# Kernel tuning notes

Measured on AMD Instinct MI355X. Metric: run time of the kernel, lower is better.

The kernel has to match this reference:

```python
import jax, jax.numpy as jnp
import numpy as np

RADIUS = 0.2
NUM_POINTS = 32
MAX_POINTS = 60
BN_EPS = 1e-5


def _bn(x, g, b, m, v):
    # BatchNorm in eval mode (running stats), channels-last broadcast
    return g * (x - m) * jax.lax.rsqrt(v + BN_EPS) + b


def setup_inputs() -> dict:
    key = jax.random.key(0)
    nk = lambda i: jax.random.fold_in(key, i)
    B, NQ, NC, HC = 2, 4096, 8192, 64
    inp = {}
    inp['p_query'] = jax.random.uniform(nk(0), (B, NQ, 3), dtype=jnp.float32)
    inp['p_context'] = jax.random.uniform(nk(1), (B, NC, 3), dtype=jnp.float32)
    inp['h_context'] = jax.random.normal(nk(2), (B, NC, HC), dtype=jnp.float32)

    def lin(i, o, ci):
        return (jax.random.normal(nk(i), (o, ci), jnp.float32) / np.sqrt(ci).astype(np.float32),
                0.01 * jax.random.normal(nk(i + 1), (o,), jnp.float32))

    def bnp(i, c):
        return (1.0 + 0.1 * jax.random.normal(nk(i), (c,), jnp.float32),
                0.1 * jax.random.normal(nk(i + 1), (c,), jnp.float32),
                0.1 * jax.random.normal(nk(i + 2), (c,), jnp.float32),
                0.5 + jax.random.uniform(nk(i + 3), (c,), jnp.float32))

    inp['w_xyz'], inp['b_xyz'] = lin(10, 64, 3)
    # pointwise 1x1 Conv2d MLP: 128 -> 128 -> 128 -> 256 (BN after each conv)
    inp['pw_w1'], inp['pw_b1'] = lin(12, 128, 128)
    inp['pw_g1'], inp['pw_be1'], inp['pw_m1'], inp['pw_v1'] = bnp(14, 128)
    inp['pw_w2'], inp['pw_b2'] = lin(20, 128, 128)
    inp['pw_g2'], inp['pw_be2'], inp['pw_m2'], inp['pw_v2'] = bnp(22, 128)
    inp['pw_w3'], inp['pw_b3'] = lin(28, 256, 128)
    inp['pw_g3'], inp['pw_be3'], inp['pw_m3'], inp['pw_v3'] = bnp(30, 256)
    # global 1x1 Conv1d MLP: 256 -> 128 -> 64 -> 3 (BN+ReLU between, none on last)
    inp['g_w1'], inp['g_b1'] = lin(36, 128, 256)
    inp['g_g1'], inp['g_be1'], inp['g_m1'], inp['g_v1'] = bnp(38, 128)
    inp['g_w2'], inp['g_b2'] = lin(44, 64, 128)
    inp['g_g2'], inp['g_be2'], inp['g_m2'], inp['g_v2'] = bnp(46, 64)
    inp['g_w3'], inp['g_b3'] = lin(52, 3, 64)
    return inp


def reference(p_query, p_context, h_context, w_xyz, b_xyz,
              pw_w1, pw_b1, pw_g1, pw_be1, pw_m1, pw_v1,
              pw_w2, pw_b2, pw_g2, pw_be2, pw_m2, pw_v2,
              pw_w3, pw_b3, pw_g3, pw_be3, pw_m3, pw_v3,
              g_w1, g_b1, g_g1, g_be1, g_m1, g_v1,
              g_w2, g_b2, g_g2, g_be2, g_m2, g_v2,
              g_w3, g_b3):
    N = p_context.shape[1]
    # knn_points: squared distances, K smallest sorted ascending
    d = (jnp.sum(p_query ** 2, -1)[:, :, None]
         - 2.0 * jnp.einsum('bqd,bnd->bqn', p_query, p_context)
         + jnp.sum(p_context ** 2, -1)[:, None, :])  # [B,NQ,NC]
    neg, idx = jax.lax.top_k(-d, MAX_POINTS)
    dist = -neg  # [B,NQ,K] ascending
    knn_idx = jnp.where(dist > RADIUS ** 2, N + 1, idx)
    idx = knn_idx[:, :, :NUM_POINTS]
    dist = dist[:, :, :NUM_POINTS]
    mask = idx == N + 1
    idx = jnp.where(mask, 0, idx)
    dist = jnp.where(mask, 0.0, dist)
    gather = jax.vmap(lambda a, i: a[i])
    pts = gather(p_context, idx)        # [B,NQ,P,3]
    h_group = gather(h_context, idx)    # [B,NQ,P,HC]
    p_rel = pts - p_query[:, :, None, :]
    h_rel = p_rel @ w_xyz.T + b_xyz     # Linear(3 -> 64)
    h = jnp.concatenate([h_rel, h_group], -1)  # [B,NQ,P,128]
    h = jax.nn.relu(_bn(h @ pw_w1.T + pw_b1, pw_g1, pw_be1, pw_m1, pw_v1))
    h = jax.nn.relu(_bn(h @ pw_w2.T + pw_b2, pw_g2, pw_be2, pw_m2, pw_v2))
    h = _bn(h @ pw_w3.T + pw_b3, pw_g3, pw_be3, pw_m3, pw_v3)  # [B,NQ,P,256]
    # cosine radius weighting (note: dist is SQUARED distance, faithful to source)
    c = 0.5 * (jnp.cos(dist * (np.pi / RADIUS)) + 1.0)
    c = jnp.where((dist <= RADIUS) & (dist > 0.0), c, 0.0)
    y = jnp.sum(h * c[..., None], axis=2)  # masked weighted pool over neighbors -> [B,NQ,256]
    y = jax.nn.relu(_bn(y @ g_w1.T + g_b1, g_g1, g_be1, g_m1, g_v1))
    y = jax.nn.relu(_bn(y @ g_w2.T + g_b2, g_g2, g_be2, g_m2, g_v2))
    return y @ g_w3.T + g_b3  # [B,NQ,3]
```

## Files before the change

### kernel.cpp

```cpp
#include <hip/hip_runtime.h>
#include <hip/hip_bf16.h>
#include <math.h>

#define BB 2
#define NQ 4096
#define NC 8192
#define KNN 32
#define WCAP 512
#define QB 4
#define MROWS 128
#define BN_EPS 1e-5f

typedef __attribute__((ext_vector_type(8))) short s16x8;
typedef __attribute__((ext_vector_type(4))) float f32x4;

#define WS_IDX   0
#define WS_CW    1048576
#define WS_Z     2097152
#define WS_SQ    6291456
#define WS_PCF   6324224
#define WS_PIDX  6586368
#define WS_CELL  6651904
#define WS_CCNT  6717440
#define WS_COFS  6718464
#define WS_W1    6719488
#define WS_W2    6752256
#define WS_W3    6785024
#define WS_GW1   6850560
#define WS_GW2   6916096
#define WS_F3    6932480
#define WS_FG1   6934528
#define WS_FG2   6935552

__device__ inline int swz(int row, int kbyte, int rb) {
    return row * rb + (kbyte ^ ((row & 7) << 4));
}
__device__ inline unsigned short f2bf(float x) {
    __hip_bfloat16 h = __float2bfloat16(x);
    return *reinterpret_cast<unsigned short*>(&h);
}
__device__ inline float bf2f(unsigned short u) {
    return __uint_as_float(((unsigned)u) << 16);
}
__device__ inline int cell1d(float x) {
    int c = (int)floorf(x * 5.0f);
    return c < 0 ? 0 : (c > 4 ? 4 : c);
}

__device__ inline void mk_img(const float* __restrict__ src, int R, int K, char* dst, int t, int NT)
{
    int rbg = (K * 2) / 16;
    int ng = R * rbg;
    for (int g = t; g < ng; g += NT) {
        int row = g / rbg;
        int b16 = (g - row * rbg) * 16;
        int sb  = b16 ^ ((row & 7) << 4);
        const float* s = src + row * K + sb / 2;
        union { s16x8 v; unsigned short u[8]; } pk;
#pragma unroll
        for (int j = 0; j < 8; ++j) pk.u[j] = f2bf(s[j]);
        *(s16x8*)(dst + row * (K * 2) + b16) = pk.v;
    }
}

__global__ __launch_bounds__(256) void prep_kernel(
    const float* __restrict__ pc,
    const float* __restrict__ w1, const float* __restrict__ w2, const float* __restrict__ w3,
    const float* __restrict__ gw1, const float* __restrict__ gw2,
    const float* __restrict__ g3, const float* __restrict__ b3, const float* __restrict__ m3,
    const float* __restrict__ v3, const float* __restrict__ be3,
    const float* __restrict__ gg1, const float* __restrict__ gb1, const float* __restrict__ gm1,
    const float* __restrict__ gv1, const float* __restrict__ gbe1,
    const float* __restrict__ gg2, const float* __restrict__ gb2, const float* __restrict__ gm2,
    const float* __restrict__ gv2, const float* __restrict__ gbe2,
    char* __restrict__ ws)
{
    const int t = blockIdx.x * 256 + threadIdx.x;
    const int NT = gridDim.x * 256;

    int* cell = (int*)(ws + WS_CELL);
    int* ccnt = (int*)(ws + WS_CCNT);
    for (int i = t; i < BB * NC; i += NT) {
        float x = pc[i*3+0], y = pc[i*3+1], z = pc[i*3+2];
        int c = (cell1d(z)*5 + cell1d(y))*5 + cell1d(x);
        cell[i] = c;
        atomicAdd(&ccnt[(i >> 13)*128 + c], 1);
    }

    mk_img(w1,  128, 128, ws + WS_W1,  t, NT);
    mk_img(w2,  128, 128, ws + WS_W2,  t, NT);
    mk_img(w3,  256, 128, ws + WS_W3,  t, NT);
    mk_img(gw1, 128, 256, ws + WS_GW1, t, NT);
    mk_img(gw2,  64, 128, ws + WS_GW2, t, NT);

    if (t < 256) {
        float s = g3[t] * rsqrtf(v3[t] + BN_EPS);
        ((float2*)(ws + WS_F3))[t] = make_float2(s, s * (b3[t] - m3[t]) + be3[t]);
    }
    if (t < 128) {
        float s = gg1[t] * rsqrtf(gv1[t] + BN_EPS);
        ((float2*)(ws + WS_FG1))[t] = make_float2(s, s * (gb1[t] - gm1[t]) + gbe1[t]);
    }
    if (t < 64) {
        float s = gg2[t] * rsqrtf(gv2[t] + BN_EPS);
        ((float2*)(ws + WS_FG2))[t] = make_float2(s, s * (gb2[t] - gm2[t]) + gbe2[t]);
    }
}

__global__ __launch_bounds__(128) void scan_kernel(char* __restrict__ ws)
{
    int* ccnt = (int*)(ws + WS_CCNT);
    int* cofs = (int*)(ws + WS_COFS);
    const int wv = threadIdx.x >> 6, lane = threadIdx.x & 63;
    const int base = wv * 128;
    int a = (lane < 125) ? ccnt[base + lane] : 0;
    int b = (64 + lane < 125) ? ccnt[base + 64 + lane] : 0;
    int ai = a, bi = b;
    for (int d = 1; d < 64; d <<= 1) {
        int t = __shfl_up(ai, d, 64);
        if (lane >= d) ai += t;
    }
    int totA = __shfl(ai, 63, 64);
    for (int d = 1; d < 64; d <<= 1) {
        int t = __shfl_up(bi, d, 64);
        if (lane >= d) bi += t;
    }
    int exA = ai - a;
    int exB = totA + bi - b;
    cofs[base + lane] = exA;       cofs[base + 64 + lane] = exB;
    ccnt[base + lane] = exA;       ccnt[base + 64 + lane] = exB;
}

__global__ __launch_bounds__(256) void scatter_kernel(
    const float* __restrict__ pc, char* __restrict__ ws)
{
    const int i = blockIdx.x * 256 + threadIdx.x;
    if (i >= BB * NC) return;
    const int b = i >> 13, loc = i & (NC - 1);
    int* cell = (int*)(ws + WS_CELL);
    int* cur  = (int*)(ws + WS_CCNT);
    float4* pcf = (float4*)(ws + WS_PCF);
    int*    pidx = (int*)(ws + WS_PIDX);
    int c = cell[i];
    int pos = atomicAdd(&cur[b*128 + c], 1);
    float x = pc[i*3+0], y = pc[i*3+1], z = pc[i*3+2];
    float w = (x*x + y*y) + z*z;
    pcf[(size_t)b*NC + pos]  = make_float4(x, y, z, w);
    pidx[(size_t)b*NC + pos] = loc;
}

__device__ inline void cmpx64(unsigned long long& k, int& p, int j, bool up) {
    unsigned long long ok = __shfl_xor(k, j, 64);
    int op = __shfl_xor(p, j, 64);
    int lane = threadIdx.x & 63;
    bool lower = (lane & j) == 0;
    bool gt = (k > ok) || (k == ok && p > op);
    bool take = (lower == up) ? gt : !gt;
    if (take) { k = ok; p = op; }
}

__device__ inline void wave_sort128(unsigned long long& k0, int& p0,
                                    unsigned long long& k1, int& p1) {
    const int lane = threadIdx.x & 63;
    for (int kk = 2; kk <= 128; kk <<= 1) {
        for (int j = kk >> 1; j > 0; j >>= 1) {
            if (j == 64) {
                bool sw = (k0 > k1) || (k0 == k1 && p0 > p1);
                if (sw) {
                    unsigned long long tk = k0; k0 = k1; k1 = tk;
                    int tp = p0; p0 = p1; p1 = tp;
                }
            } else {
                bool up0 = ((lane & kk) == 0);
                bool up1 = (kk == 128) ? true : ((kk == 64) ? false : up0);
                cmpx64(k0, p0, j, up0);
                cmpx64(k1, p1, j, up1);
            }
        }
    }
}

__global__ __launch_bounds__(256) void knn_kernel(
    const float* __restrict__ pq, const float* __restrict__ pc,
    const float4* __restrict__ pcf, const int* __restrict__ pidx,
    const int* __restrict__ cofs,
    int* __restrict__ idx_out, float* __restrict__ cw_out)
{
    __shared__ unsigned long long kbuf[4][WCAP];
    __shared__ int pbuf[4][WCAP];

    const int tid = threadIdx.x, lane = tid & 63, w = tid >> 6;
    const int gq = blockIdx.x * 4 + w;
    const int b = gq >> 12;

    const float qxf = pq[gq*3+0], qyf = pq[gq*3+1], qzf = pq[gq*3+2];
    const double qx = (double)qxf, qy = (double)qyf, qz = (double)qzf;
    const double sq = qx*qx + qy*qy + qz*qz;
    const float  sqf = (float)sq;
    const double R2d = 0.2 * 0.2;
    const float  R2f = 0.04f + 1e-4f;

    const float4* pcfb = pcf + (size_t)b * NC;
    const int*    pidb = pidx + (size_t)b * NC;
    const int*    cb   = cofs + b * 128;
    const float*  pcb  = pc + (size_t)b * NC * 3;

    int xlo = (int)floorf((qxf - 0.2f) * 5.0f - 1e-3f); xlo = xlo < 0 ? 0 : xlo;
    int xhi = (int)floorf((qxf + 0.2f) * 5.0f + 1e-3f); xhi = xhi > 4 ? 4 : xhi;
    int ylo = (int)floorf((qyf - 0.2f) * 5.0f - 1e-3f); ylo = ylo < 0 ? 0 : ylo;
    int yhi = (int)floorf((qyf + 0.2f) * 5.0f + 1e-3f); yhi = yhi > 4 ? 4 : yhi;
    int zlo = (int)floorf((qzf - 0.2f) * 5.0f - 1e-3f); zlo = zlo < 0 ? 0 : zlo;
    int zhi = (int)floorf((qzf + 0.2f) * 5.0f + 1e-3f); zhi = zhi > 4 ? 4 : zhi;

    const unsigned long long lt = (lane == 63) ? ~0ULL >> 1 : (1ULL << lane) - 1;
    int cnt = 0;
    for (int zi = zlo; zi <= zhi; ++zi) {
        for (int yi = ylo; yi <= yhi; ++yi) {
            int row = (zi*5 + yi)*5;
            int s = cb[row + xlo], e = cb[row + xhi + 1];
            for (int t0 = s; t0 < e; t0 += 64) {
                int t = t0 + lane;
                bool pred = false;
                int pidv = 0;
                if (t < e) {
                    float4 cd = pcfb[t];
                    float dot = (qxf*cd.x + qyf*cd.y) + qzf*cd.z;
                    float d   = (sqf - 2.0f*dot) + cd.w;
                    pred = (d <= R2f);
                    if (pred) pidv = pidb[t];
                }
                unsigned long long mask = __ballot(pred);
                if (pred) {
                    int pos = cnt + __popcll(mask & lt);
                    if (pos < WCAP) pbuf[w][pos] = pidv;
                }
                cnt += __popcll(mask);
            }
        }
    }
    if (cnt > WCAP) cnt = WCAP;

    for (int i = lane; i < cnt; i += 64) {
        int n = pbuf[w][i];
        double cx = (double)pcb[n*3+0];
        double cy = (double)pcb[n*3+1];
        double cz = (double)pcb[n*3+2];
        double dot = qx*cx + qy*cy + qz*cz;
        double sc  = cx*cx + cy*cy + cz*cz;
        double d   = (sq - 2.0*dot) + sc;
        if (d <= R2d) {
            double dc = d < 0.0 ? 0.0 : d;
            kbuf[w][i] = (unsigned long long)__double_as_longlong(dc);
        } else {
            kbuf[w][i] = ~0ULL;
            pbuf[w][i] = 0x7fffffff;
        }
    }

    unsigned long long k0 = (lane < cnt)      ? kbuf[w][lane]      : ~0ULL;
    unsigned long long k1 = (64 + lane < cnt) ? kbuf[w][64 + lane] : ~0ULL;
    int p0 = (lane < cnt)      ? pbuf[w][lane]      : 0x7fffffff;
    int p1 = (64 + lane < cnt) ? pbuf[w][64 + lane] : 0x7fffffff;
    wave_sort128(k0, p0, k1, p1);
    int consumed = 128;
    while (consumed < cnt) {
        if (lane >= 32) {
            int i0 = consumed + lane - 32;
            k0 = (i0 < cnt) ? kbuf[w][i0] : ~0ULL;
            p0 = (i0 < cnt) ? pbuf[w][i0] : 0x7fffffff;
        }
        int i1 = consumed + 32 + lane;
        k1 = (i1 < cnt) ? kbuf[w][i1] : ~0ULL;
        p1 = (i1 < cnt) ? pbuf[w][i1] : 0x7fffffff;
        wave_sort128(k0, p0, k1, p1);
        consumed += 96;
    }

    if (lane < KNN) {
        int id = 0; float c = 0.0f;
        if (k0 != ~0ULL) {
            id = p0;
            double d = __longlong_as_double((long long)k0);
            if (d > 0.0 && d <= 0.2) {
                double cw = 0.5 * (cos(d * 15.707963267948966) + 1.0);
                c = (float)cw;
            }
        }
        idx_out[gq*KNN + lane] = id;
        cw_out[gq*KNN + lane]  = c;
    }
}

__global__ __launch_bounds__(512, 4) void front_kernel(
    const float* __restrict__ pq, const float* __restrict__ pc, const float* __restrict__ hc,
    const float* __restrict__ w_xyz, const float* __restrict__ b_xyz,
    const float* __restrict__ b1, const float* __restrict__ g1,
    const float* __restrict__ be1, const float* __restrict__ m1, const float* __restrict__ v1,
    const float* __restrict__ b2, const float* __restrict__ g2,
    const float* __restrict__ be2, const float* __restrict__ m2, const float* __restrict__ v2,
    const char* __restrict__ w1img, const char* __restrict__ w2img,
    const int* __restrict__ idx_in, const float* __restrict__ cw_in,
    float* __restrict__ z_buf, float* __restrict__ sq_buf)
{
    __shared__ __align__(16) char smem[70144];
    char*  Ab   = smem;
    char*  Wb   = smem + 32768;
    float* Prel = (float*)(smem + 65536);
    float* Cw   = (float*)(smem + 67072);
    int*   Sidx = (int*)  (smem + 67584);
    float* Sfd  = (float*)(smem + 68096);

    const int tid = threadIdx.x;
    const int qbase = blockIdx.x * QB;
    const int b = qbase >> 12;
    const float* pcb = pc + (size_t)b * NC * 3;
    const float* hcb = hc + (size_t)b * NC * 64;

    if (tid < MROWS) {
        int id = idx_in[qbase*KNN + tid];
        Sidx[tid] = id;
        Cw[tid]   = cw_in[qbase*KNN + tid];
        int gq = qbase + (tid >> 5);
        Prel[tid*3+0] = pcb[id*3+0] - pq[gq*3+0];
        Prel[tid*3+1] = pcb[id*3+1] - pq[gq*3+1];
        Prel[tid*3+2] = pcb[id*3+2] - pq[gq*3+2];
    }
    __syncthreads();

    for (int p = tid; p < MROWS*16; p += 512) {
        int row = p >> 4, seg = p & 15;
        float vals[8];
        if (seg >= 8) {
            const float* src = hcb + (size_t)Sidx[row]*64 + (seg-8)*8;
            float4 u0 = *(const float4*)src;
            float4 u1 = *(const float4*)(src+4);
            vals[0]=u0.x; vals[1]=u0.y; vals[2]=u0.z; vals[3]=u0.w;
            vals[4]=u1.x; vals[5]=u1.y; vals[6]=u1.z; vals[7]=u1.w;
        } else {
            float px = Prel[row*3+0], py = Prel[row*3+1], pz = Prel[row*3+2];
            int c0 = seg*8;
#pragma unroll
            for (int j = 0; j < 8; ++j) {
                int c = c0 + j;
                vals[j] = px*w_xyz[c*3+0] + py*w_xyz[c*3+1] + pz*w_xyz[c*3+2] + b_xyz[c];
            }
        }
        union { s16x8 v; unsigned short u[8]; } pk;
#pragma unroll
        for (int j = 0; j < 8; ++j) pk.u[j] = f2bf(vals[j]);
        *(s16x8*)(Ab + swz(row, seg*16, 256)) = pk.v;
    }
    if (tid < 128) {
        int j = tid;
        float s0 = g1[j] * rsqrtf(v1[j] + BN_EPS);
        Sfd[0*128 + j] = s0; Sfd[1*128 + j] = s0*(b1[j]-m1[j]) + be1[j];
        float s1 = g2[j] * rsqrtf(v2[j] + BN_EPS);
        Sfd[2*128 + j] = s1; Sfd[3*128 + j] = s1*(b2[j]-m2[j]) + be2[j];
    }
    if (tid < QB) {
        float s = 0.0f;
        for (int i = 0; i < KNN; ++i) s += Cw[tid*KNN + i];
        sq_buf[qbase + tid] = s;
    }

    const int l = tid & 63, w = tid >> 6;
    const int r0 = w * 16, cl = l & 15, q4 = l >> 4;

#pragma unroll 1
    for (int L = 0; L < 2; ++L) {
        const s16x8* wimg = (const s16x8*)(L ? w2img : w1img);
        s16x8* Wv = (s16x8*)Wb;
        for (int p = tid; p < 2048; p += 512) Wv[p] = wimg[p];
        __syncthreads();

        f32x4 acc[8];
#pragma unroll
        for (int nt = 0; nt < 8; ++nt) acc[nt] = (f32x4){0.f,0.f,0.f,0.f};
#pragma unroll
        for (int kk = 0; kk < 4; ++kk) {
            int kbyte = kk*64 + q4*16;
            s16x8 a0 = *(const s16x8*)(Ab + swz(r0 + cl, kbyte, 256));
#pragma unroll
            for (int nt = 0; nt < 8; ++nt) {
                s16x8 bwv = *(const s16x8*)(Wb + swz(nt*16 + cl, kbyte, 256));
                acc[nt] = __builtin_amdgcn_mfma_f32_16x16x32_bf16(a0, bwv, acc[nt], 0, 0, 0);
            }
        }
#pragma unroll
        for (int nt = 0; nt < 8; ++nt) {
            int j = nt*16 + cl;
            float s = Sfd[(L*2+0)*128 + j], t = Sfd[(L*2+1)*128 + j];
#pragma unroll
            for (int r = 0; r < 4; ++r) {
                int row = r0 + q4*4 + r;
                float x = fmaxf(acc[nt][r]*s + t, 0.0f);
                *(unsigned short*)(Ab + swz(row, j*2, 256)) = f2bf(x);
            }
        }
        __syncthreads();
    }

    {
        int q = tid >> 7, col = tid & 127;
        float s = 0.0f;
#pragma unroll
        for (int i = 0; i < KNN; ++i) {
            unsigned short u = *(const unsigned short*)(Ab + swz(q*KNN + i, col*2, 256));
            s += Cw[q*KNN + i] * bf2f(u);
        }
        z_buf[(size_t)(qbase + q)*128 + col] = s;
    }
}

__global__ __launch_bounds__(256) void tail_kernel(
    const char* __restrict__ w3img, const char* __restrict__ gw1img, const char* __restrict__ gw2img,
    const float2* __restrict__ f3, const float2* __restrict__ fg1, const float2* __restrict__ fg2,
    const float* __restrict__ z_buf, const float* __restrict__ sq_buf,
    const float* __restrict__ gw3, const float* __restrict__ gb3,
    float* __restrict__ out)
{
    __shared__ __align__(16) char smem[123136];
    char* A1 = smem;
    char* A2 = smem + 16384;
    char* A4 = smem + 49152;
    char* Wb = smem + 57344;
    float* Ssm = (float*)(smem + 122880);

    const int tid = threadIdx.x;
    const int q0 = blockIdx.x * 64;

    for (int g = tid; g < 1024; g += 256) {
        int row = g >> 4, seg = g & 15;
        const float* zs = z_buf + (size_t)(q0 + row)*128 + seg*8;
        float4 u0 = *(const float4*)zs;
        float4 u1 = *(const float4*)(zs+4);
        union { s16x8 v; unsigned short u[8]; } pk;
        pk.u[0]=f2bf(u0.x); pk.u[1]=f2bf(u0.y); pk.u[2]=f2bf(u0.z); pk.u[3]=f2bf(u0.w);
        pk.u[4]=f2bf(u1.x); pk.u[5]=f2bf(u1.y); pk.u[6]=f2bf(u1.z); pk.u[7]=f2bf(u1.w);
        *(s16x8*)(A1 + swz(row, seg*16, 256)) = pk.v;
    }
    for (int p = tid; p < 4096; p += 256) ((s16x8*)Wb)[p] = ((const s16x8*)w3img)[p];
    if (tid < 64) Ssm[tid] = sq_buf[q0 + tid];
    __syncthreads();

    const int l = tid & 63, w = tid >> 6;
    const int r0 = w*16, cl = l & 15, q4 = l >> 4;

    {
        f32x4 acc[16];
#pragma unroll
        for (int nt = 0; nt < 16; ++nt) acc[nt] = (f32x4){0.f,0.f,0.f,0.f};
#pragma unroll
        for (int kk = 0; kk < 4; ++kk) {
            int kbyte = kk*64 + q4*16;
            s16x8 a0 = *(const s16x8*)(A1 + swz(r0 + cl, kbyte, 256));
#pragma unroll
            for (int nt = 0; nt < 16; ++nt) {
                s16x8 bwv = *(const s16x8*)(Wb + swz(nt*16 + cl, kbyte, 256));
                acc[nt] = __builtin_amdgcn_mfma_f32_16x16x32_bf16(a0, bwv, acc[nt], 0, 0, 0);
            }
        }
#pragma unroll
        for (int nt = 0; nt < 16; ++nt) {
            int j = nt*16 + cl;
            float2 f = f3[j];
#pragma unroll
            for (int r = 0; r < 4; ++r) {
                int row = r0 + q4*4 + r;
                float S = Ssm[row];
                float x = f.x*acc[nt][r] + S*f.y;
                *(unsigned short*)(A2 + swz(row, j*2, 512)) = f2bf(x);
            }
        }
    }
    __syncthreads();
    for (int p = tid; p < 4096; p += 256) ((s16x8*)Wb)[p] = ((const s16x8*)gw1img)[p];
    __syncthreads();

    {
        f32x4 acc[8];
#pragma unroll
        for (int nt = 0; nt < 8; ++nt) acc[nt] = (f32x4){0.f,0.f,0.f,0.f};
#pragma unroll
        for (int kk = 0; kk < 8; ++kk) {
            int kbyte = kk*64 + q4*16;
            s16x8 a0 = *(const s16x8*)(A2 + swz(r0 + cl, kbyte, 512));
#pragma unroll
            for (int nt = 0; nt < 8; ++nt) {
                s16x8 bwv = *(const s16x8*)(Wb + swz(nt*16 + cl, kbyte, 512));
                acc[nt] = __builtin_amdgcn_mfma_f32_16x16x32_bf16(a0, bwv, acc[nt], 0, 0, 0);
            }
        }
#pragma unroll
        for (int nt = 0; nt < 8; ++nt) {
            int j = nt*16 + cl;
            float2 f = fg1[j];
#pragma unroll
            for (int r = 0; r < 4; ++r) {
                int row = r0 + q4*4 + r;
                float x = fmaxf(f.x*acc[nt][r] + f.y, 0.0f);
                *(unsigned short*)(A1 + swz(row, j*2, 256)) = f2bf(x);
            }
        }
    }
    __syncthreads();
    for (int p = tid; p < 1024; p += 256) ((s16x8*)Wb)[p] = ((const s16x8*)gw2img)[p];
    __syncthreads();

    {
        f32x4 acc[4];
#pragma unroll
        for (int nt = 0; nt < 4; ++nt) acc[nt] = (f32x4){0.f,0.f,0.f,0.f};
#pragma unroll
        for (int kk = 0; kk < 4; ++kk) {
            int kbyte = kk*64 + q4*16;
            s16x8 a0 = *(const s16x8*)(A1 + swz(r0 + cl, kbyte, 256));
#pragma unroll
            for (int nt = 0; nt < 4; ++nt) {
                s16x8 bwv = *(const s16x8*)(Wb + swz(nt*16 + cl, kbyte, 256));
                acc[nt] = __builtin_amdgcn_mfma_f32_16x16x32_bf16(a0, bwv, acc[nt], 0, 0, 0);
            }
        }
#pragma unroll
        for (int nt = 0; nt < 4; ++nt) {
            int j = nt*16 + cl;
            float2 f = fg2[j];
#pragma unroll
            for (int r = 0; r < 4; ++r) {
                int row = r0 + q4*4 + r;
                float x = fmaxf(f.x*acc[nt][r] + f.y, 0.0f);
                *(unsigned short*)(A4 + swz(row, j*2, 128)) = f2bf(x);
            }
        }
    }
    __syncthreads();

    if (tid < 192) {
        int q = tid / 3, jj = tid - q*3;
        const float* wr = gw3 + jj*64;
        float s = 0.0f;
        for (int k = 0; k < 64; ++k) {
            unsigned short u = *(const unsigned short*)(A4 + swz(q, k*2, 128));
            s += bf2f(u) * wr[k];
        }
        out[(size_t)(q0 + q)*3 + jj] = s + gb3[jj];
    }
}

extern "C" void kernel_launch(void* const* d_in, const int* in_sizes, int n_in,
                              void* d_out, int out_size, void* d_ws, size_t ws_size,
                              hipStream_t stream)
{
    const float* pq    = (const float*)d_in[0];
    const float* pc    = (const float*)d_in[1];
    const float* hc    = (const float*)d_in[2];
    const float* w_xyz = (const float*)d_in[3];
    const float* b_xyz = (const float*)d_in[4];
    const float* w1    = (const float*)d_in[5];
    const float* b1    = (const float*)d_in[6];
    const float* g1    = (const float*)d_in[7];
    const float* be1   = (const float*)d_in[8];
    const float* m1    = (const float*)d_in[9];
    const float* v1    = (const float*)d_in[10];
    const float* w2    = (const float*)d_in[11];
    const float* b2    = (const float*)d_in[12];
    const float* g2    = (const float*)d_in[13];
    const float* be2   = (const float*)d_in[14];
    const float* m2    = (const float*)d_in[15];
    const float* v2    = (const float*)d_in[16];
    const float* w3    = (const float*)d_in[17];
    const float* b3    = (const float*)d_in[18];
    const float* g3    = (const float*)d_in[19];
    const float* be3   = (const float*)d_in[20];
    const float* m3    = (const float*)d_in[21];
    const float* v3    = (const float*)d_in[22];
    const float* gw1   = (const float*)d_in[23];
    const float* gb1   = (const float*)d_in[24];
    const float* gg1   = (const float*)d_in[25];
    const float* gbe1  = (const float*)d_in[26];
    const float* gm1   = (const float*)d_in[27];
    const float* gv1   = (const float*)d_in[28];
    const float* gw2   = (const float*)d_in[29];
    const float* gb2   = (const float*)d_in[30];
    const float* gg2   = (const float*)d_in[31];
    const float* gbe2  = (const float*)d_in[32];
    const float* gm2   = (const float*)d_in[33];
    const float* gv2   = (const float*)d_in[34];
    const float* gw3   = (const float*)d_in[35];
    const float* gb3   = (const float*)d_in[36];

    char* ws = (char*)d_ws;
    int*   idx_buf = (int*)(ws + WS_IDX);
    float* cw_buf  = (float*)(ws + WS_CW);
    float* z_buf   = (float*)(ws + WS_Z);
    float* sq_buf  = (float*)(ws + WS_SQ);

    hipMemsetAsync(ws + WS_CCNT, 0, 1024, stream);

    prep_kernel<<<64, 256, 0, stream>>>(pc, w1, w2, w3, gw1, gw2,
        g3, b3, m3, v3, be3, gg1, gb1, gm1, gv1, gbe1, gg2, gb2, gm2, gv2, gbe2, ws);

    scan_kernel<<<1, 128, 0, stream>>>(ws);

    scatter_kernel<<<(BB*NC + 255)/256, 256, 0, stream>>>(pc, ws);

    knn_kernel<<<(BB*NQ)/4, 256, 0, stream>>>(pq, pc,
        (const float4*)(ws + WS_PCF), (const int*)(ws + WS_PIDX),
        (const int*)(ws + WS_COFS), idx_buf, cw_buf);

    front_kernel<<<(BB*NQ)/QB, 512, 0, stream>>>(pq, pc, hc, w_xyz, b_xyz,
        b1, g1, be1, m1, v1, b2, g2, be2, m2, v2,
        ws + WS_W1, ws + WS_W2, idx_buf, cw_buf, z_buf, sq_buf);

    tail_kernel<<<(BB*NQ)/64, 256, 0, stream>>>(
        ws + WS_W3, ws + WS_GW1, ws + WS_GW2,
        (const float2*)(ws + WS_F3), (const float2*)(ws + WS_FG1), (const float2*)(ws + WS_FG2),
        z_buf, sq_buf, gw3, gb3, (float*)d_out);
}
```

Measured before the change: 171.2 us.

## Pack float distance and index into one key; select top-64 before double-precision rescoring

The KNN kernel now packs the float squared distance and point index into a single 64-bit key when collecting candidates. It sorts these with a key-only bitonic sort plus merge, keeping the 64 smallest. Only those 64 survivors are rescored in double precision and re-sorted as key/index pairs, which removes the separate index buffer and most of the per-candidate double math and paired shuffles. The risk is that float-precision preselection could drop a true neighbour near the rank-32 boundary, though keeping 64 candidates leaves margin.

Result: faster. 144.5 us, median of 2 (-15.6%).

```diff
diff --git a/kernel.cpp b/kernel.cpp
--- a/kernel.cpp
+++ b/kernel.cpp
@@ -149,35 +149,42 @@
     pidx[(size_t)b*NC + pos] = loc;
 }
 
+__device__ inline void cmpxu(unsigned long long& k, int j, bool up) {
+    unsigned long long ok = __shfl_xor(k, j, 64);
+    bool lower = ((threadIdx.x & 63) & j) == 0;
+    bool take = (lower == up) ? (k > ok) : (k < ok);
+    if (take) k = ok;
+}
+__device__ inline void sortasc64(unsigned long long& k) {
+    const int lane = threadIdx.x & 63;
+    for (int kk = 2; kk <= 64; kk <<= 1)
+        for (int j = kk >> 1; j > 0; j >>= 1)
+            cmpxu(k, j, (lane & kk) == 0);
+}
+__device__ inline void sortdesc64(unsigned long long& k) {
+    const int lane = threadIdx.x & 63;
+    for (int kk = 2; kk <= 64; kk <<= 1)
+        for (int j = kk >> 1; j > 0; j >>= 1)
+            cmpxu(k, j, (lane & kk) != 0);
+}
+__device__ inline void merge128(unsigned long long& k0, unsigned long long& k1) {
+    if (k0 > k1) { unsigned long long t = k0; k0 = k1; k1 = t; }
+#pragma unroll
+    for (int j = 32; j > 0; j >>= 1) { cmpxu(k0, j, true); cmpxu(k1, j, true); }
+}
 __device__ inline void cmpx64(unsigned long long& k, int& p, int j, bool up) {
     unsigned long long ok = __shfl_xor(k, j, 64);
     int op = __shfl_xor(p, j, 64);
-    int lane = threadIdx.x & 63;
-    bool lower = (lane & j) == 0;
+    bool lower = ((threadIdx.x & 63) & j) == 0;
     bool gt = (k > ok) || (k == ok && p > op);
     bool take = (lower == up) ? gt : !gt;
     if (take) { k = ok; p = op; }
 }
-
-__device__ inline void wave_sort128(unsigned long long& k0, int& p0,
-                                    unsigned long long& k1, int& p1) {
+__device__ inline void sortasc64kp(unsigned long long& k, int& p) {
     const int lane = threadIdx.x & 63;
-    for (int kk = 2; kk <= 128; kk <<= 1) {
-        for (int j = kk >> 1; j > 0; j >>= 1) {
-            if (j == 64) {
-                bool sw = (k0 > k1) || (k0 == k1 && p0 > p1);
-                if (sw) {
-                    unsigned long long tk = k0; k0 = k1; k1 = tk;
-                    int tp = p0; p0 = p1; p1 = tp;
-                }
-            } else {
-                bool up0 = ((lane & kk) == 0);
-                bool up1 = (kk == 128) ? true : ((kk == 64) ? false : up0);
-                cmpx64(k0, p0, j, up0);
-                cmpx64(k1, p1, j, up1);
-            }
-        }
-    }
+    for (int kk = 2; kk <= 64; kk <<= 1)
+        for (int j = kk >> 1; j > 0; j >>= 1)
+            cmpx64(k, p, j, (lane & kk) == 0);
 }
 
 __global__ __launch_bounds__(256) void knn_kernel(
@@ -187,7 +194,6 @@
     int* __restrict__ idx_out, float* __restrict__ cw_out)
 {
     __shared__ unsigned long long kbuf[4][WCAP];
-    __shared__ int pbuf[4][WCAP];
 
     const int tid = threadIdx.x, lane = tid & 63, w = tid >> 6;
     const int gq = blockIdx.x * 4 + w;
@@ -221,18 +227,22 @@
             for (int t0 = s; t0 < e; t0 += 64) {
                 int t = t0 + lane;
                 bool pred = false;
-                int pidv = 0;
+                unsigned long long key = ~0ULL;
                 if (t < e) {
                     float4 cd = pcfb[t];
                     float dot = (qxf*cd.x + qyf*cd.y) + qzf*cd.z;
                     float d   = (sqf - 2.0f*dot) + cd.w;
                     pred = (d <= R2f);
-                    if (pred) pidv = pidb[t];
+                    if (pred) {
+                        float dc = fmaxf(d, 0.0f);
+                        key = ((unsigned long long)__float_as_uint(dc) << 32)
+                            | (unsigned)pidb[t];
+                    }
                 }
                 unsigned long long mask = __ballot(pred);
                 if (pred) {
                     int pos = cnt + __popcll(mask & lt);
-                    if (pos < WCAP) pbuf[w][pos] = pidv;
+                    if (pos < WCAP) kbuf[w][pos] = key;
                 }
                 cnt += __popcll(mask);
             }
@@ -240,8 +250,24 @@
     }
     if (cnt > WCAP) cnt = WCAP;
 
-    for (int i = lane; i < cnt; i += 64) {
-        int n = pbuf[w][i];
+    unsigned long long k0 = (lane < cnt)      ? kbuf[w][lane]      : ~0ULL;
+    unsigned long long k1 = (64 + lane < cnt) ? kbuf[w][64 + lane] : ~0ULL;
+    sortasc64(k0);
+    sortdesc64(k1);
+    merge128(k0, k1);
+    int consumed = 128;
+    while (consumed < cnt) {
+        int i1 = consumed + lane;
+        k1 = (i1 < cnt) ? kbuf[w][i1] : ~0ULL;
+        sortdesc64(k1);
+        merge128(k0, k1);
+        consumed += 64;
+    }
+
+    unsigned long long kf = ~0ULL;
+    int pf = 0x7fffffff;
+    if (k0 != ~0ULL) {
+        int n = (int)(k0 & 0xffffffffULL);
         double cx = (double)pcb[n*3+0];
         double cy = (double)pcb[n*3+1];
         double cz = (double)pcb[n*3+2];
@@ -250,37 +276,17 @@
         double d   = (sq - 2.0*dot) + sc;
         if (d <= R2d) {
             double dc = d < 0.0 ? 0.0 : d;
-            kbuf[w][i] = (unsigned long long)__double_as_longlong(dc);
-        } else {
-            kbuf[w][i] = ~0ULL;
-            pbuf[w][i] = 0x7fffffff;
-        }
-    }
-
-    unsigned long long k0 = (lane < cnt)      ? kbuf[w][lane]      : ~0ULL;
-    unsigned long long k1 = (64 + lane < cnt) ? kbuf[w][64 + lane] : ~0ULL;
-    int p0 = (lane < cnt)      ? pbuf[w][lane]      : 0x7fffffff;
-    int p1 = (64 + lane < cnt) ? pbuf[w][64 + lane] : 0x7fffffff;
-    wave_sort128(k0, p0, k1, p1);
-    int consumed = 128;
-    while (consumed < cnt) {
-        if (lane >= 32) {
-            int i0 = consumed + lane - 32;
-            k0 = (i0 < cnt) ? kbuf[w][i0] : ~0ULL;
-            p0 = (i0 < cnt) ? pbuf[w][i0] : 0x7fffffff;
-        }
-        int i1 = consumed + 32 + lane;
-        k1 = (i1 < cnt) ? kbuf[w][i1] : ~0ULL;
-        p1 = (i1 < cnt) ? pbuf[w][i1] : 0x7fffffff;
-        wave_sort128(k0, p0, k1, p1);
-        consumed += 96;
-    }
+            kf = (unsigned long long)__double_as_longlong(dc);
+            pf = n;
+        }
+    }
+    sortasc64kp(kf, pf);
 
     if (lane < KNN) {
         int id = 0; float c = 0.0f;
-        if (k0 != ~0ULL) {
-            id = p0;
-            double d = __longlong_as_double((long long)k0);
+        if (kf != ~0ULL) {
+            id = pf;
+            double d = __longlong_as_double((long long)kf);
             if (d > 0.0 && d <= 0.2) {
                 double cw = 0.5 * (cos(d * 15.707963267948966) + 1.0);
                 c = (float)cw;
```
